# Kernel tuning notes

Hardware: AMD Instinct MI355X
Metric: run time of the kernel (lower is better)

Reference implementation:

```python
import jax, jax.numpy as jnp
import numpy as np

BBOX_W, CAP_W, OBJ_W = 5.0, 0.1, 1.0
BIG = 1e9
EPS = 1e-7

def _norm_boxes(b):
    # ensure x1<=x2, y1<=y2
    x1 = jnp.minimum(b[..., 0], b[..., 2]); y1 = jnp.minimum(b[..., 1], b[..., 3])
    x2 = jnp.maximum(b[..., 0], b[..., 2]); y2 = jnp.maximum(b[..., 1], b[..., 3])
    return jnp.stack([x1, y1, x2, y2], axis=-1)

def _giou(b1, b2):
    b1 = _norm_boxes(b1); b2 = _norm_boxes(b2)
    xi1 = jnp.maximum(b1[..., 0], b2[..., 0]); yi1 = jnp.maximum(b1[..., 1], b2[..., 1])
    xi2 = jnp.minimum(b1[..., 2], b2[..., 2]); yi2 = jnp.minimum(b1[..., 3], b2[..., 3])
    inter = jnp.clip(xi2 - xi1, 0.0) * jnp.clip(yi2 - yi1, 0.0)
    a1 = (b1[..., 2] - b1[..., 0]) * (b1[..., 3] - b1[..., 1])
    a2 = (b2[..., 2] - b2[..., 0]) * (b2[..., 3] - b2[..., 1])
    union = a1 + a2 - inter
    iou = inter / (union + EPS)
    xe1 = jnp.minimum(b1[..., 0], b2[..., 0]); ye1 = jnp.minimum(b1[..., 1], b2[..., 1])
    xe2 = jnp.maximum(b1[..., 2], b2[..., 2]); ye2 = jnp.maximum(b1[..., 3], b2[..., 3])
    enc = (xe2 - xe1) * (ye2 - ye1)
    return iou - (enc - union) / (enc + EPS)

def _greedy_match(cost):
    # deterministic jit-safe assignment: repeatedly pick global min of cost (N,M)
    N, M = cost.shape
    def step(carry, _):
        ru, cu = carry  # used-row / used-col masks
        c = cost + BIG * ru[:, None] + BIG * cu[None, :]
        f = jnp.argmin(c)
        i, j = f // M, f % M
        return (ru.at[i].set(1.0), cu.at[j].set(1.0)), (i, j)
    _, (pis, gjs) = jax.lax.scan(step, (jnp.zeros(N), jnp.zeros(M)), None, length=M)
    return pis, gjs  # each (M,) int

def _per_sample(pb, po, cl, gb, gt):
    # fused pairwise cost matrix (N,M): L1 + (1-GIoU) + objectness cost
    l1 = jnp.abs(pb[:, None, :] - gb[None, :, :]).sum(-1)
    g = _giou(pb[:, None, :], gb[None, :, :])
    cost = l1 + (1.0 - g) + (1.0 - jax.nn.sigmoid(po))[:, None]
    pis, gjs = _greedy_match(jax.lax.stop_gradient(cost))
    mp, mg = pb[pis], gb[gjs]
    l1_loss = jnp.abs(mp - mg).mean()
    giou_loss = jnp.clip((1.0 - _giou(mp, mg)).mean(), 0.0, 2.0)
    bbox = jnp.clip(l1_loss + giou_loss, 0.0)
    # objectness BCE-with-logits over all N predictions
    t = jnp.zeros_like(po).at[pis].set(1.0)
    obj = (jnp.maximum(po, 0.0) - po * t + jnp.log1p(jnp.exp(-jnp.abs(po)))).mean()
    obj = jnp.clip(obj, 0.0)
    # caption next-token CE: logits[:L-1] predict tokens[1:L]
    ml = cl[pis]                    # (M, L, V)
    tgt = gt[gjs][:, 1:]            # (M, L-1)
    logp = jax.nn.log_softmax(ml[:, :-1, :], axis=-1)
    ce = -jnp.take_along_axis(logp, tgt[..., None], axis=-1)[..., 0].mean(-1)
    cap = jnp.clip(jnp.clip(ce, 0.0).mean(), 0.0)
    return bbox, cap, obj

def reference(pred_boxes, pred_objectness, caption_logits, gt_boxes, gt_tokens):
    bbox, cap, obj = jax.vmap(_per_sample)(pred_boxes, pred_objectness, caption_logits, gt_boxes, gt_tokens)
    total = jnp.clip((BBOX_W * bbox + CAP_W * cap + OBJ_W * obj).mean(), 0.0)
    comps = jax.lax.stop_gradient(jnp.stack([BBOX_W * bbox.mean(), CAP_W * cap.mean(), OBJ_W * obj.mean()]))
    return jnp.concatenate([total[None], comps])  # (4,)

def setup_inputs() -> dict:
    key = jax.random.key(0)
    k1, k2, k3, k4, k5 = jax.random.split(key, 5)
    B, N, M, L, V = 2, 256, 32, 16, 32000
    return {
        'pred_boxes': jax.random.uniform(k1, (B, N, 4), dtype=jnp.float32),
        'pred_objectness': jax.random.normal(k2, (B, N), dtype=jnp.float32),
        'caption_logits': jax.random.normal(k3, (B, N, L, V), dtype=jnp.float32),
        'gt_boxes': jax.random.uniform(k4, (B, M, 4), dtype=jnp.float32),
        'gt_tokens': jax.random.randint(k5, (B, M, L), 0, V, dtype=jnp.int64) if jax.config.jax_enable_x64 else jax.random.randint(k5, (B, M, L), 0, V, dtype=jnp.int32),
    }
```

## Files before the change

kernel.cpp:

```cpp
#include <hip/hip_runtime.h>
#include <math.h>

#define B_SZ 2
#define N_PRED 256
#define M_GT 32
#define L_TOK 16
#define V_VOCAB 32000
#define P_POS 15
#define NROW 960
#define ROW4 8000
#define MAGIC 0x5A5A5A5Au

__device__ __forceinline__ float giou_f(float4 b1, float4 b2) {
    float ax1 = fminf(b1.x, b1.z), ay1 = fminf(b1.y, b1.w);
    float ax2 = fmaxf(b1.x, b1.z), ay2 = fmaxf(b1.y, b1.w);
    float bx1 = fminf(b2.x, b2.z), by1 = fminf(b2.y, b2.w);
    float bx2 = fmaxf(b2.x, b2.z), by2 = fmaxf(b2.y, b2.w);
    float xi1 = fmaxf(ax1, bx1), yi1 = fmaxf(ay1, by1);
    float xi2 = fminf(ax2, bx2), yi2 = fminf(ay2, by2);
    float inter = fmaxf(xi2 - xi1, 0.f) * fmaxf(yi2 - yi1, 0.f);
    float a1 = (ax2 - ax1) * (ay2 - ay1);
    float a2 = (bx2 - bx1) * (by2 - by1);
    float uni = a1 + a2 - inter;
    float iou = inter / (uni + 1e-7f);
    float xe1 = fminf(ax1, bx1), ye1 = fminf(ay1, by1);
    float xe2 = fmaxf(ax2, bx2), ye2 = fmaxf(ay2, by2);
    float enc = (xe2 - xe1) * (ye2 - ye1);
    return iou - (enc - uni) / (enc + 1e-7f);
}

#define DPP_MIN(ctrl, rmask)                                               \
    {                                                                      \
        unsigned nv = (unsigned)__builtin_amdgcn_update_dpp(               \
            (int)0xFFFFFFFF, (int)scan, (ctrl), (rmask), 0xF, false);      \
        if (nv < scan) scan = nv;                                          \
    }

__device__ __forceinline__ void fold4(float4 v, float& m, float& s) {
    float m4 = fmaxf(fmaxf(v.x, v.y), fmaxf(v.z, v.w));
    float mn = fmaxf(m, m4);
    s = s * __expf(m - mn) +
        __expf(v.x - mn) + __expf(v.y - mn) +
        __expf(v.z - mn) + __expf(v.w - mn);
    m = mn;
}

__global__ __launch_bounds__(256) void matchcap_kernel(
    const float* __restrict__ pred_boxes, const float* __restrict__ pred_obj,
    const float* __restrict__ cl,         const float* __restrict__ gt_boxes,
    const int* __restrict__ gt_tokens,
    int* __restrict__ pis, int* __restrict__ gjs,
    float* __restrict__ bbox_ws, float* __restrict__ obj_ws,
    float* __restrict__ ce, unsigned* __restrict__ flags)
{
    const int tid = threadIdx.x;
    const int wv  = tid >> 6;
    const int ln  = tid & 63;

    if (blockIdx.x < 2) {
        const int b = blockIdx.x;
        __shared__ float4 gbS[M_GT];
        __shared__ float4 pbS[N_PRED];
        __shared__ unsigned long long wkeyd[2][4];
        __shared__ float wosum[4];

        if (tid < M_GT) gbS[tid] = ((const float4*)gt_boxes)[b * M_GT + tid];
        const float4 pp = ((const float4*)pred_boxes)[b * N_PRED + tid];
        const float  po = pred_obj[b * N_PRED + tid];
        pbS[tid] = pp;
        __syncthreads();

        const float objc = 1.f - 1.f / (1.f + __expf(-po));
        float cr[M_GT];
        float bestv = INFINITY; int bestj = 0;
#pragma unroll
        for (int j = 0; j < M_GT; ++j) {
            float4 g = gbS[j];
            float l1 = fabsf(pp.x - g.x) + fabsf(pp.y - g.y) +
                       fabsf(pp.z - g.z) + fabsf(pp.w - g.w);
            float c = l1 + (1.f - giou_f(pp, g)) + objc;
            cr[j] = c;
            if (c < bestv) { bestv = c; bestj = j; }
        }

        unsigned colUsed = 0;
        bool rowUsed = false;
        int my_pi = 0, my_gj = 0;

        for (int t = 0; t < M_GT; ++t) {
            const unsigned cand = rowUsed ? 0xFFFFFFFFu : __float_as_uint(bestv);
            const int      flat = tid * M_GT + bestj;
            unsigned scan = cand;
            DPP_MIN(0x111, 0xF);
            DPP_MIN(0x112, 0xF);
            DPP_MIN(0x114, 0xF);
            DPP_MIN(0x118, 0xF);
            DPP_MIN(0x142, 0xA);
            DPP_MIN(0x143, 0xC);
            const unsigned vmin = (unsigned)__builtin_amdgcn_readlane((int)scan, 63);
            const unsigned long long mk = __ballot(cand == vmin);
            const int srcl  = __ffsll(mk) - 1;
            const int flatw = __builtin_amdgcn_readlane(flat, srcl);
            if (ln == 0)
                wkeyd[t & 1][wv] = ((unsigned long long)vmin << 32) | (unsigned)flatw;
            __syncthreads();
            const unsigned long long* wk = wkeyd[t & 1];
            unsigned long long g0 = wk[0] < wk[1] ? wk[0] : wk[1];
            unsigned long long g1 = wk[2] < wk[3] ? wk[2] : wk[3];
            unsigned long long g  = g0 < g1 ? g0 : g1;
            const int gflat = (int)(g & 0x1FFFu);
            const int wi = gflat >> 5;
            const int wj = gflat & 31;
            if (tid == t)  { my_pi = wi; my_gj = wj; }
            if (tid == wi) rowUsed = true;
            colUsed |= 1u << wj;
            if (!rowUsed && bestj == wj) {
                float bv = INFINITY; int bj = 0;
#pragma unroll
                for (int j = 0; j < M_GT; ++j) {
                    float c = ((colUsed >> j) & 1) ? INFINITY : cr[j];
                    if (c < bv) { bv = c; bj = j; }
                }
                bestv = bv; bestj = bj;
            }
        }

        if (tid < M_GT) {
            pis[b * M_GT + tid] = my_pi;
            gjs[b * M_GT + tid] = my_gj;
        }

        float l1sum = 0.f, gsum = 0.f;
        if (tid < M_GT) {
            float4 mp = pbS[my_pi];
            float4 mg = gbS[my_gj];
            l1sum = fabsf(mp.x - mg.x) + fabsf(mp.y - mg.y) +
                    fabsf(mp.z - mg.z) + fabsf(mp.w - mg.w);
            gsum = 1.f - giou_f(mp, mg);
        }
        float osum = fmaxf(po, 0.f) - po * (rowUsed ? 1.f : 0.f) +
                     log1pf(__expf(-fabsf(po)));
        for (int off = 32; off > 0; off >>= 1) {
            l1sum += __shfl_xor(l1sum, off);
            gsum  += __shfl_xor(gsum,  off);
            osum  += __shfl_xor(osum,  off);
        }
        if (ln == 0) wosum[wv] = osum;
        __syncthreads();
        if (tid == 0) {
            float l1_loss   = l1sum / 128.f;
            float giou_loss = fminf(fmaxf(gsum / 32.f, 0.f), 2.f);
            bbox_ws[b] = fmaxf(l1_loss + giou_loss, 0.f);
            float ot = wosum[0] + wosum[1] + wosum[2] + wosum[3];
            obj_ws[b]  = fmaxf(ot / 256.f, 0.f);
        }
        __syncthreads();
        __threadfence();
        if (tid == 0)
            __hip_atomic_store(&flags[b], MAGIC, __ATOMIC_RELEASE,
                               __HIP_MEMORY_SCOPE_AGENT);
        return;
    }

    const int r   = blockIdx.x - 2;
    const int b   = r / (M_GT * P_POS);
    const int rem = r % (M_GT * P_POS);
    const int k   = rem / P_POS;
    const int p   = rem % P_POS;

    if (tid == 0) {
        while (__hip_atomic_load(&flags[0], __ATOMIC_ACQUIRE,
                                 __HIP_MEMORY_SCOPE_AGENT) != MAGIC ||
               __hip_atomic_load(&flags[1], __ATOMIC_ACQUIRE,
                                 __HIP_MEMORY_SCOPE_AGENT) != MAGIC)
            __builtin_amdgcn_s_sleep(2);
    }
    __syncthreads();

    const int n = pis[b * M_GT + k];
    const float* row = cl + ((size_t)(b * N_PRED + n) * L_TOK + p) * V_VOCAB;
    const float4* row4 = (const float4*)row;

    float m0 = -INFINITY, s0 = 0.f;
    float m1 = -INFINITY, s1 = 0.f;
    for (int idx = tid; idx < ROW4; idx += 512) {
        fold4(row4[idx], m0, s0);
        int i2 = idx + 256;
        if (i2 < ROW4) fold4(row4[i2], m1, s1);
    }
    float m = fmaxf(m0, m1);
    float s = s0 * __expf(m0 - m) + s1 * __expf(m1 - m);

    for (int off = 32; off > 0; off >>= 1) {
        float mo = __shfl_xor(m, off);
        float so = __shfl_xor(s, off);
        float mm = fmaxf(m, mo);
        s = s * __expf(m - mm) + so * __expf(mo - mm);
        m = mm;
    }

    __shared__ float wm[4], wsum[4];
    if (ln == 0) { wm[wv] = m; wsum[wv] = s; }
    __syncthreads();
    if (tid == 0) {
        float mm = fmaxf(fmaxf(wm[0], wm[1]), fmaxf(wm[2], wm[3]));
        float st = wsum[0] * __expf(wm[0] - mm) + wsum[1] * __expf(wm[1] - mm) +
                   wsum[2] * __expf(wm[2] - mm) + wsum[3] * __expf(wm[3] - mm);
        const int gj  = gjs[b * M_GT + k];
        const int tgt = gt_tokens[(b * M_GT + gj) * L_TOK + (p + 1)];
        ce[r] = mm + __logf(st) - row[tgt];
    }
}

__global__ __launch_bounds__(64) void finalize_kernel(
    const float* __restrict__ ce, const float* __restrict__ bbox,
    const float* __restrict__ obj, float* __restrict__ out)
{
    const int l = threadIdx.x;
    float sum = 0.f;
#pragma unroll
    for (int q = 0; q < P_POS; ++q) sum += ce[l * P_POS + q];
    float cek = fmaxf(sum / (float)P_POS, 0.f);
    for (int off = 16; off > 0; off >>= 1) cek += __shfl_xor(cek, off);
    float cap_b = fmaxf(cek / (float)M_GT, 0.f);
    float cap0 = __shfl(cap_b, 0);
    float cap1 = __shfl(cap_b, 32);
    if (l == 0) {
        float bb0 = bbox[0], bb1 = bbox[1];
        float ob0 = obj[0],  ob1 = obj[1];
        float per0 = 5.f * bb0 + 0.1f * cap0 + ob0;
        float per1 = 5.f * bb1 + 0.1f * cap1 + ob1;
        out[0] = fmaxf(0.5f * (per0 + per1), 0.f);
        out[1] = 5.f  * 0.5f * (bb0 + bb1);
        out[2] = 0.1f * 0.5f * (cap0 + cap1);
        out[3] = 0.5f * (ob0 + ob1);
    }
}

extern "C" void kernel_launch(void* const* d_in, const int* in_sizes, int n_in,
                              void* d_out, int out_size, void* d_ws, size_t ws_size,
                              hipStream_t stream) {
    const float* pred_boxes = (const float*)d_in[0];
    const float* pred_obj   = (const float*)d_in[1];
    const float* cap_logits = (const float*)d_in[2];
    const float* gt_boxes   = (const float*)d_in[3];
    const int*   gt_tokens  = (const int*)d_in[4];
    float* out = (float*)d_out;

    int*      pis   = (int*)d_ws;
    int*      gjs   = pis + B_SZ * M_GT;
    float*    bbox  = (float*)(gjs + B_SZ * M_GT);
    float*    obj   = bbox + B_SZ;
    float*    ce    = obj + B_SZ;
    unsigned* flags = (unsigned*)(ce + NROW);

    matchcap_kernel<<<2 + NROW, 256, 0, stream>>>(
        pred_boxes, pred_obj, cap_logits, gt_boxes, gt_tokens,
        pis, gjs, bbox, obj, ce, flags);
    finalize_kernel<<<1, 64, 0, stream>>>(ce, bbox, obj, out);
}
```

Baseline: 61.66 us.

## Fuse finalize reduction into main kernel via tagged-value polling

```diff
diff --git a/kernel.cpp b/kernel.cpp
--- a/kernel.cpp
+++ b/kernel.cpp
@@ -8,6 +8,7 @@
 #define V_VOCAB 32000
 #define P_POS 15
 #define NROW 960
+#define NGRP 64
 #define ROW4 8000
 #define MAGIC 0x5A5A5A5Au
 
@@ -45,13 +46,28 @@
     m = mn;
 }
 
-__global__ __launch_bounds__(256) void matchcap_kernel(
+__device__ __forceinline__ void publish(unsigned long long* p, float v) {
+    unsigned long long t =
+        ((unsigned long long)MAGIC << 32) | (unsigned long long)__float_as_uint(v);
+    __hip_atomic_store(p, t, __ATOMIC_RELAXED, __HIP_MEMORY_SCOPE_AGENT);
+}
+__device__ __forceinline__ float pollv(const unsigned long long* p) {
+    unsigned long long v;
+    while (((v = __hip_atomic_load(p, __ATOMIC_RELAXED,
+                                   __HIP_MEMORY_SCOPE_AGENT)) >> 32) != MAGIC)
+        __builtin_amdgcn_s_sleep(2);
+    return __uint_as_float((unsigned)v);
+}
+
+__global__ __launch_bounds__(256) void fused_detloss_kernel(
     const float* __restrict__ pred_boxes, const float* __restrict__ pred_obj,
     const float* __restrict__ cl,         const float* __restrict__ gt_boxes,
     const int* __restrict__ gt_tokens,
     int* __restrict__ pis, int* __restrict__ gjs,
-    float* __restrict__ bbox_ws, float* __restrict__ obj_ws,
-    float* __restrict__ ce, unsigned* __restrict__ flags)
+    unsigned long long* __restrict__ ce64,
+    unsigned long long* __restrict__ grp64,
+    unsigned long long* __restrict__ bo64,
+    unsigned* __restrict__ flags, float* __restrict__ out)
 {
     const int tid = threadIdx.x;
     const int wv  = tid >> 6;
@@ -150,9 +166,9 @@
         if (tid == 0) {
             float l1_loss   = l1sum / 128.f;
             float giou_loss = fminf(fmaxf(gsum / 32.f, 0.f), 2.f);
-            bbox_ws[b] = fmaxf(l1_loss + giou_loss, 0.f);
+            publish(&bo64[b],     fmaxf(l1_loss + giou_loss, 0.f));
             float ot = wosum[0] + wosum[1] + wosum[2] + wosum[3];
-            obj_ws[b]  = fmaxf(ot / 256.f, 0.f);
+            publish(&bo64[2 + b], fmaxf(ot / 256.f, 0.f));
         }
         __syncthreads();
         __threadfence();
@@ -167,6 +183,7 @@
     const int rem = r % (M_GT * P_POS);
     const int k   = rem / P_POS;
     const int p   = rem % P_POS;
+    const int l   = r / P_POS;
 
     if (tid == 0) {
         while (__hip_atomic_load(&flags[0], __ATOMIC_ACQUIRE,
@@ -200,34 +217,44 @@
     }
 
     __shared__ float wm[4], wsum[4];
+    __shared__ float pollS[NGRP + 4];
     if (ln == 0) { wm[wv] = m; wsum[wv] = s; }
     __syncthreads();
+
+    float cev = 0.f;
     if (tid == 0) {
         float mm = fmaxf(fmaxf(wm[0], wm[1]), fmaxf(wm[2], wm[3]));
         float st = wsum[0] * __expf(wm[0] - mm) + wsum[1] * __expf(wm[1] - mm) +
                    wsum[2] * __expf(wm[2] - mm) + wsum[3] * __expf(wm[3] - mm);
         const int gj  = gjs[b * M_GT + k];
         const int tgt = gt_tokens[(b * M_GT + gj) * L_TOK + (p + 1)];
-        ce[r] = mm + __logf(st) - row[tgt];
-    }
-}
-
-__global__ __launch_bounds__(64) void finalize_kernel(
-    const float* __restrict__ ce, const float* __restrict__ bbox,
-    const float* __restrict__ obj, float* __restrict__ out)
-{
-    const int l = threadIdx.x;
-    float sum = 0.f;
-#pragma unroll
-    for (int q = 0; q < P_POS; ++q) sum += ce[l * P_POS + q];
-    float cek = fmaxf(sum / (float)P_POS, 0.f);
-    for (int off = 16; off > 0; off >>= 1) cek += __shfl_xor(cek, off);
-    float cap_b = fmaxf(cek / (float)M_GT, 0.f);
-    float cap0 = __shfl(cap_b, 0);
-    float cap1 = __shfl(cap_b, 32);
-    if (l == 0) {
-        float bb0 = bbox[0], bb1 = bbox[1];
-        float ob0 = obj[0],  ob1 = obj[1];
+        cev = mm + __logf(st) - row[tgt];
+        publish(&ce64[r], cev);
+    }
+    if (p != 0) return;
+
+    if (tid >= 1 && tid < P_POS)
+        pollS[tid] = pollv(&ce64[l * P_POS + tid]);
+    __syncthreads();
+    if (tid == 0) {
+        float sum = cev;
+        for (int q = 1; q < P_POS; ++q) sum += pollS[q];
+        publish(&grp64[l], fmaxf(sum / (float)P_POS, 0.f));
+    }
+    if (r != 0) return;
+
+    __syncthreads();
+    if (tid < NGRP)           pollS[tid] = pollv(&grp64[tid]);
+    else if (tid < NGRP + 4)  pollS[tid] = pollv(&bo64[tid - NGRP]);
+    __syncthreads();
+    if (tid == 0) {
+        float c0 = 0.f, c1 = 0.f;
+        for (int q = 0; q < 32; ++q)  c0 += pollS[q];
+        for (int q = 32; q < 64; ++q) c1 += pollS[q];
+        float cap0 = fmaxf(c0 / 32.f, 0.f);
+        float cap1 = fmaxf(c1 / 32.f, 0.f);
+        float bb0 = pollS[NGRP + 0], bb1 = pollS[NGRP + 1];
+        float ob0 = pollS[NGRP + 2], ob1 = pollS[NGRP + 3];
         float per0 = 5.f * bb0 + 0.1f * cap0 + ob0;
         float per1 = 5.f * bb1 + 0.1f * cap1 + ob1;
         out[0] = fmaxf(0.5f * (per0 + per1), 0.f);
@@ -247,15 +274,14 @@
     const int*   gt_tokens  = (const int*)d_in[4];
     float* out = (float*)d_out;
 
-    int*      pis   = (int*)d_ws;
+    unsigned long long* ce64  = (unsigned long long*)d_ws;
+    unsigned long long* grp64 = ce64 + NROW;
+    unsigned long long* bo64  = grp64 + NGRP;
+    int*      pis   = (int*)(bo64 + 4);
     int*      gjs   = pis + B_SZ * M_GT;
-    float*    bbox  = (float*)(gjs + B_SZ * M_GT);
-    float*    obj   = bbox + B_SZ;
-    float*    ce    = obj + B_SZ;
-    unsigned* flags = (unsigned*)(ce + NROW);
-
-    matchcap_kernel<<<2 + NROW, 256, 0, stream>>>(
+    unsigned* flags = (unsigned*)(gjs + B_SZ * M_GT);
+
+    fused_detloss_kernel<<<2 + NROW, 256, 0, stream>>>(
         pred_boxes, pred_obj, cap_logits, gt_boxes, gt_tokens,
-        pis, gjs, bbox, obj, ce, flags);
-    finalize_kernel<<<1, 64, 0, stream>>>(ce, bbox, obj, out);
-}
+        pis, gjs, ce64, grp64, bo64, flags, out);
+}
```

Result: no change. 60.91 us (-1.2%).
